# Kernel optimization log

Measured on AMD Instinct MI355X. Metric: run time of the kernel, lower is better.

The kernel has to match this reference:

```python
import jax, jax.numpy as jnp
import numpy as np

N_NODES = 100000
DIM_IN = 128
DIM_OUT = 128
N_EDGES = 1600000
EPS = 0.0  # PyG GINConv default, non-trainable


def setup_inputs() -> dict:
    key = jax.random.key(0)
    k1, k2, k3, k4, k5, k6 = jax.random.split(key, 6)
    node_feature = jax.random.normal(k1, (N_NODES, DIM_IN), dtype=jnp.float32)
    edge_index = jax.random.randint(k2, (2, N_EDGES), 0, N_NODES, dtype=jnp.int64)
    s1 = 1.0 / np.sqrt(DIM_IN)
    s2 = 1.0 / np.sqrt(DIM_OUT)
    W1 = jax.random.uniform(k3, (DIM_IN, DIM_OUT), jnp.float32, -s1, s1)
    b1 = jax.random.uniform(k4, (DIM_OUT,), jnp.float32, -s1, s1)
    W2 = jax.random.uniform(k5, (DIM_OUT, DIM_OUT), jnp.float32, -s2, s2)
    b2 = jax.random.uniform(k6, (DIM_OUT,), jnp.float32, -s2, s2)
    return {"node_feature": node_feature, "edge_index": edge_index,
            "W1": W1, "b1": b1, "W2": W2, "b2": b2}


def reference(node_feature, edge_index, W1, b1, W2, b2):
    src, dst = edge_index[0], edge_index[1]
    # scatter-add neighbor aggregation: messages x_j = x[src] summed at dst
    agg = jax.ops.segment_sum(node_feature[src], dst, num_segments=N_NODES)  # [N, d]
    h = (1.0 + EPS) * node_feature + agg
    h = jax.nn.relu(h @ W1 + b1)
    return h @ W2 + b2
```

## Files before the change

kernel.cpp:

```cpp
#include <hip/hip_runtime.h>

#define NN 100000
#define D  128
#define NE 1600000

#define NBK2 782
#define CAP2 2816
#define EPB  8192
#define NFB  196
#define ENTCAP 2048

typedef __bf16 bf16x8 __attribute__((ext_vector_type(8)));
typedef __bf16 bf16x4 __attribute__((ext_vector_type(4)));
typedef float  f32x4  __attribute__((ext_vector_type(4)));

__global__ __launch_bounds__(256)
void init_kernel(const float* __restrict__ W1, const float* __restrict__ W2,
                 __bf16* __restrict__ w1t, __bf16* __restrict__ w2t,
                 int* __restrict__ gcur) {
    const int bid = blockIdx.x;
    const int tid = threadIdx.x;
    if (bid < 128) {
        int i = bid * 256 + tid;
        if (i < 16384) {
            int c = i >> 7, k = i & 127;
            w1t[i] = (__bf16)W1[k * 128 + c];
        } else {
            int j = i - 16384;
            int c = j >> 7, k = j & 127;
            w2t[j] = (__bf16)W2[k * 128 + c];
        }
    } else {
        int i = (bid - 128) * 256 + tid;
        if (i < NBK2) gcur[i] = 0;
    }
}

__global__ __launch_bounds__(512)
void fill2x_kernel(const float* __restrict__ x, const int* __restrict__ ei,
                   int* __restrict__ gcur, __bf16* __restrict__ xb,
                   int* __restrict__ bedge) {
    __shared__ int            stage[EPB];
    __shared__ unsigned short bid16[EPB];
    __shared__ int            lofs[NBK2];
    __shared__ int            lpos[NBK2];
    __shared__ int            gbase[NBK2];
    __shared__ int            ssum[512];
    __shared__ int            tot;

    const int tid = threadIdx.x;
    const int e0  = blockIdx.x * EPB;

    for (int b = tid; b < NBK2; b += 512) lpos[b] = 0;
    __syncthreads();

    int eb[16], epk[16];
    #pragma unroll 16
    for (int k = 0; k < 16; ++k) {
        int e = e0 + k * 512 + tid;
        eb[k] = -1;
        if (e < NE) {
            int s = ei[e];
            int d = ei[NE + e];
            if ((unsigned)s < NN && (unsigned)d < NN) {
                eb[k]  = d >> 7;
                epk[k] = ((d & 127) << 17) | s;
                atomicAdd(&lpos[eb[k]], 1);
            }
        }
    }

    for (int i = blockIdx.x * 512 + tid; i < NN * 32; i += NFB * 512) {
        float4 v = reinterpret_cast<const float4*>(x)[i];
        bf16x4 o = {(__bf16)v.x, (__bf16)v.y, (__bf16)v.z, (__bf16)v.w};
        reinterpret_cast<bf16x4*>(xb)[i] = o;
    }
    __syncthreads();

    int t2 = tid * 2;
    int c0 = (t2 < NBK2) ? lpos[t2] : 0;
    int c1 = (t2 + 1 < NBK2) ? lpos[t2 + 1] : 0;
    ssum[tid] = c0 + c1;
    __syncthreads();
    for (int off = 1; off < 512; off <<= 1) {
        int v = (tid >= off) ? ssum[tid - off] : 0;
        __syncthreads();
        ssum[tid] += v;
        __syncthreads();
    }
    int excl = ssum[tid] - (c0 + c1);
    if (t2 < NBK2) {
        lofs[t2] = excl;
        lpos[t2] = excl;
        if (c0) gbase[t2] = atomicAdd(&gcur[t2], c0);
    }
    if (t2 + 1 < NBK2) {
        lofs[t2 + 1] = excl + c0;
        lpos[t2 + 1] = excl + c0;
        if (c1) gbase[t2 + 1] = atomicAdd(&gcur[t2 + 1], c1);
    }
    if (tid == 511) tot = ssum[511];
    __syncthreads();

    #pragma unroll 16
    for (int k = 0; k < 16; ++k) {
        if (eb[k] >= 0) {
            int r = atomicAdd(&lpos[eb[k]], 1);
            stage[r] = epk[k];
            bid16[r] = (unsigned short)eb[k];
        }
    }
    __syncthreads();

    int T = tot;
    for (int i = tid; i < T; i += 512) {
        int b   = bid16[i];
        int pos = gbase[b] + (i - lofs[b]);
        if (pos < CAP2) bedge[b * CAP2 + pos] = stage[i];
    }
}

__global__ __launch_bounds__(256)
void gather3_kernel(const __bf16* __restrict__ xb, const int* __restrict__ gcur,
                    const int* __restrict__ bedge, __bf16* __restrict__ hb) {
    __shared__ int ent[ENTCAP];
    __shared__ int c64[64], ofs[65], cur[64], scn[64];

    const int b    = blockIdx.x >> 1;
    const int half = blockIdx.x & 1;
    const int tid  = threadIdx.x;

    int cnt = gcur[b]; if (cnt > CAP2) cnt = CAP2;
    const int base = b * CAP2;

    if (tid < 64) c64[tid] = 0;
    __syncthreads();

    for (int i = tid; i < cnt; i += 256) {
        int v  = bedge[base + i];
        int dl = v >> 17;
        if ((dl >> 6) == half) atomicAdd(&c64[dl & 63], 1);
    }
    __syncthreads();

    if (tid < 64) scn[tid] = c64[tid];
    __syncthreads();
    #pragma unroll
    for (int off = 1; off < 64; off <<= 1) {
        int v = (tid >= off && tid < 64) ? scn[tid - off] : 0;
        __syncthreads();
        if (tid < 64) scn[tid] += v;
        __syncthreads();
    }
    if (tid < 64) {
        ofs[tid + 1] = scn[tid];
        if (tid == 0) ofs[0] = 0;
        cur[tid] = scn[tid] - c64[tid];
    }
    __syncthreads();

    for (int i = tid; i < cnt; i += 256) {
        int v  = bedge[base + i];
        int dl = v >> 17;
        if ((dl >> 6) == half) {
            int r = atomicAdd(&cur[dl & 63], 1);
            if (r < ENTCAP) ent[r] = v & 0x1FFFF;
        }
    }
    __syncthreads();

    const int wave   = tid >> 6;
    const int lane   = tid & 63;
    const int half32 = lane >> 5;
    const int l31    = lane & 31;
    const bf16x4* xv4 = reinterpret_cast<const bf16x4*>(xb);

    for (int q = wave; q < 64; q += 4) {
        int node = b * 128 + half * 64 + q;
        if (node >= NN) continue;
        int beg = ofs[q], end = ofs[q + 1];
        if (beg > ENTCAP) beg = ENTCAP;
        if (end > ENTCAP) end = ENTCAP;

        float a0 = 0.f, a1 = 0.f, a2 = 0.f, a3 = 0.f;
        float b0 = 0.f, b1 = 0.f, b2f = 0.f, b3 = 0.f;
        int j = beg;
        for (; j + 4 <= end; j += 4) {
            int s0 = ent[j + half32];
            int s1 = ent[j + 2 + half32];
            bf16x4 v0 = xv4[(size_t)s0 * 32 + l31];
            bf16x4 v1 = xv4[(size_t)s1 * 32 + l31];
            a0 += (float)v0[0]; a1 += (float)v0[1];
            a2 += (float)v0[2]; a3 += (float)v0[3];
            b0 += (float)v1[0]; b1 += (float)v1[1];
            b2f += (float)v1[2]; b3 += (float)v1[3];
        }
        if (j + 2 <= end) {
            int s0 = ent[j + half32];
            bf16x4 v0 = xv4[(size_t)s0 * 32 + l31];
            a0 += (float)v0[0]; a1 += (float)v0[1];
            a2 += (float)v0[2]; a3 += (float)v0[3];
            j += 2;
        }
        if (j < end && half32 == 0) {
            int s0 = ent[j];
            bf16x4 v0 = xv4[(size_t)s0 * 32 + l31];
            a0 += (float)v0[0]; a1 += (float)v0[1];
            a2 += (float)v0[2]; a3 += (float)v0[3];
        }
        a0 += b0; a1 += b1; a2 += b2f; a3 += b3;
        a0 += __shfl_xor(a0, 32); a1 += __shfl_xor(a1, 32);
        a2 += __shfl_xor(a2, 32); a3 += __shfl_xor(a3, 32);

        if (half32 == 0) {
            bf16x4 sv = xv4[(size_t)node * 32 + l31];
            bf16x4 o = {(__bf16)(a0 + (float)sv[0]), (__bf16)(a1 + (float)sv[1]),
                        (__bf16)(a2 + (float)sv[2]), (__bf16)(a3 + (float)sv[3])};
            reinterpret_cast<bf16x4*>(hb)[(size_t)node * 32 + l31] = o;
        }
    }
}

__global__ __launch_bounds__(512)
void mlp2_kernel(const __bf16* __restrict__ hb,
                 const __bf16* __restrict__ w1t,
                 const __bf16* __restrict__ w2t,
                 const float* __restrict__ b1,
                 const float* __restrict__ b2,
                 float* __restrict__ out) {
    __shared__ __align__(16) unsigned char sh_h[128 * 256];

    const int tid  = threadIdx.x;
    const int row0 = blockIdx.x * 128;

    for (int c = tid; c < 2048; c += 512) {
        int r = c >> 4, s = c & 15;
        int grow = row0 + r;
        int4 val = make_int4(0, 0, 0, 0);
        if (grow < NN) val = *reinterpret_cast<const int4*>(hb + (size_t)grow * 128 + s * 8);
        *reinterpret_cast<int4*>(sh_h + r * 256 + ((s * 16) ^ ((r & 7) << 4))) = val;
    }
    __syncthreads();

    const int wave  = tid >> 6;
    const int lane  = tid & 63;
    const int wr    = wave >> 2;
    const int wc    = wave & 3;
    const int l15   = lane & 15;
    const int kbyte = (lane >> 4) * 16;
    const int kelem = (lane >> 4) * 8;

    bf16x8 bf[2][4];
    #pragma unroll
    for (int nn = 0; nn < 2; ++nn) {
        int col = wc * 32 + nn * 16 + l15;
        #pragma unroll
        for (int ks = 0; ks < 4; ++ks)
            bf[nn][ks] = *reinterpret_cast<const bf16x8*>(
                w1t + col * 128 + ks * 32 + kelem);
    }

    f32x4 acc[4][2];
    #pragma unroll
    for (int m = 0; m < 4; ++m) {
        acc[m][0] = f32x4{0.f, 0.f, 0.f, 0.f};
        acc[m][1] = f32x4{0.f, 0.f, 0.f, 0.f};
        int row = wr * 64 + m * 16 + l15;
        bf16x8 af[4];
        #pragma unroll
        for (int ks = 0; ks < 4; ++ks)
            af[ks] = *reinterpret_cast<const bf16x8*>(
                sh_h + row * 256 + ((ks * 64 + kbyte) ^ ((row & 7) << 4)));
        #pragma unroll
        for (int ks = 0; ks < 4; ++ks) {
            acc[m][0] = __builtin_amdgcn_mfma_f32_16x16x32_bf16(af[ks], bf[0][ks], acc[m][0], 0, 0, 0);
            acc[m][1] = __builtin_amdgcn_mfma_f32_16x16x32_bf16(af[ks], bf[1][ks], acc[m][1], 0, 0, 0);
        }
    }

    float bias1a = b1[wc * 32 + l15];
    float bias1b = b1[wc * 32 + 16 + l15];

    __syncthreads();

    #pragma unroll
    for (int m = 0; m < 4; ++m) {
        #pragma unroll
        for (int nn = 0; nn < 2; ++nn) {
            int col = wc * 32 + nn * 16 + l15;
            float bb = nn ? bias1b : bias1a;
            #pragma unroll
            for (int j = 0; j < 4; ++j) {
                int row = wr * 64 + m * 16 + (lane >> 4) * 4 + j;
                float v = fmaxf(acc[m][nn][j] + bb, 0.f);
                *reinterpret_cast<__bf16*>(
                    sh_h + row * 256 + ((col * 2) ^ ((row & 7) << 4))) = (__bf16)v;
            }
        }
    }
    __syncthreads();

    #pragma unroll
    for (int nn = 0; nn < 2; ++nn) {
        int col = wc * 32 + nn * 16 + l15;
        #pragma unroll
        for (int ks = 0; ks < 4; ++ks)
            bf[nn][ks] = *reinterpret_cast<const bf16x8*>(
                w2t + col * 128 + ks * 32 + kelem);
    }

    f32x4 acc2[4][2];
    #pragma unroll
    for (int m = 0; m < 4; ++m) {
        acc2[m][0] = f32x4{0.f, 0.f, 0.f, 0.f};
        acc2[m][1] = f32x4{0.f, 0.f, 0.f, 0.f};
        int row = wr * 64 + m * 16 + l15;
        bf16x8 af[4];
        #pragma unroll
        for (int ks = 0; ks < 4; ++ks)
            af[ks] = *reinterpret_cast<const bf16x8*>(
                sh_h + row * 256 + ((ks * 64 + kbyte) ^ ((row & 7) << 4)));
        #pragma unroll
        for (int ks = 0; ks < 4; ++ks) {
            acc2[m][0] = __builtin_amdgcn_mfma_f32_16x16x32_bf16(af[ks], bf[0][ks], acc2[m][0], 0, 0, 0);
            acc2[m][1] = __builtin_amdgcn_mfma_f32_16x16x32_bf16(af[ks], bf[1][ks], acc2[m][1], 0, 0, 0);
        }
    }

    float bias2a = b2[wc * 32 + l15];
    float bias2b = b2[wc * 32 + 16 + l15];
    #pragma unroll
    for (int m = 0; m < 4; ++m) {
        #pragma unroll
        for (int nn = 0; nn < 2; ++nn) {
            int col = wc * 32 + nn * 16 + l15;
            float bb = nn ? bias2b : bias2a;
            #pragma unroll
            for (int j = 0; j < 4; ++j) {
                int row = row0 + wr * 64 + m * 16 + (lane >> 4) * 4 + j;
                if (row < NN) out[(size_t)row * 128 + col] = acc2[m][nn][j] + bb;
            }
        }
    }
}

extern "C" void kernel_launch(void* const* d_in, const int* in_sizes, int n_in,
                              void* d_out, int out_size, void* d_ws, size_t ws_size,
                              hipStream_t stream) {
    const float* x  = (const float*)d_in[0];
    const int*   ei = (const int*)d_in[1];
    const float* W1 = (const float*)d_in[2];
    const float* b1 = (const float*)d_in[3];
    const float* W2 = (const float*)d_in[4];
    const float* b2 = (const float*)d_in[5];
    float* out = (float*)d_out;

    int* gcur  = (int*)d_ws;
    int* bedge = gcur + NBK2;
    size_t int_end = (size_t)(NBK2 + (size_t)NBK2 * CAP2) * 4;
    size_t bf_off  = (int_end + 255) & ~(size_t)255;
    __bf16* xb  = (__bf16*)((char*)d_ws + bf_off);
    __bf16* hb  = xb + (size_t)NN * D;
    __bf16* w1t = hb + (size_t)NN * D;
    __bf16* w2t = w1t + D * D;

    init_kernel<<<132, 256, 0, stream>>>(W1, W2, w1t, w2t, gcur);
    fill2x_kernel<<<NFB, 512, 0, stream>>>(x, ei, gcur, xb, bedge);
    gather3_kernel<<<NBK2 * 2, 256, 0, stream>>>(xb, gcur, bedge, hb);
    mlp2_kernel<<<NBK2, 512, 0, stream>>>(hb, w1t, w2t, b1, b2, out);
}
```

Measured before the change: 137.5 us.

## Fuse neighbor gather with two-layer MLP in a single kernel

The gather kernel now writes each block's 64 aggregated rows straight into shared memory in the swizzled layout and runs both MFMA GEMM layers on that tile in the same block. This removes the bf16 intermediate buffer, its global write and re-read, and one kernel launch. In exchange each block holds more shared memory and registers, and it does GEMM work with only 4 waves over 64 rows, so the MLP phase may use fewer MFMA units at once and overlap less with gather latency.

After: 155.3 us. 1.13x slower.

```diff
diff --git a/kernel.cpp b/kernel.cpp
--- a/kernel.cpp
+++ b/kernel.cpp
@@ -121,10 +121,16 @@
 }
 
 __global__ __launch_bounds__(256)
-void gather3_kernel(const __bf16* __restrict__ xb, const int* __restrict__ gcur,
-                    const int* __restrict__ bedge, __bf16* __restrict__ hb) {
+void gather_mlp_kernel(const __bf16* __restrict__ xb, const int* __restrict__ gcur,
+                       const int* __restrict__ bedge,
+                       const __bf16* __restrict__ w1t,
+                       const __bf16* __restrict__ w2t,
+                       const float* __restrict__ b1,
+                       const float* __restrict__ b2,
+                       float* __restrict__ out) {
     __shared__ int ent[ENTCAP];
     __shared__ int c64[64], ofs[65], cur[64], scn[64];
+    __shared__ __align__(16) unsigned char sh_h[64 * 256];
 
     const int b    = blockIdx.x >> 1;
     const int half = blockIdx.x & 1;
@@ -177,75 +183,54 @@
 
     for (int q = wave; q < 64; q += 4) {
         int node = b * 128 + half * 64 + q;
-        if (node >= NN) continue;
-        int beg = ofs[q], end = ofs[q + 1];
-        if (beg > ENTCAP) beg = ENTCAP;
-        if (end > ENTCAP) end = ENTCAP;
-
         float a0 = 0.f, a1 = 0.f, a2 = 0.f, a3 = 0.f;
-        float b0 = 0.f, b1 = 0.f, b2f = 0.f, b3 = 0.f;
-        int j = beg;
-        for (; j + 4 <= end; j += 4) {
-            int s0 = ent[j + half32];
-            int s1 = ent[j + 2 + half32];
-            bf16x4 v0 = xv4[(size_t)s0 * 32 + l31];
-            bf16x4 v1 = xv4[(size_t)s1 * 32 + l31];
-            a0 += (float)v0[0]; a1 += (float)v0[1];
-            a2 += (float)v0[2]; a3 += (float)v0[3];
-            b0 += (float)v1[0]; b1 += (float)v1[1];
-            b2f += (float)v1[2]; b3 += (float)v1[3];
-        }
-        if (j + 2 <= end) {
-            int s0 = ent[j + half32];
-            bf16x4 v0 = xv4[(size_t)s0 * 32 + l31];
-            a0 += (float)v0[0]; a1 += (float)v0[1];
-            a2 += (float)v0[2]; a3 += (float)v0[3];
-            j += 2;
-        }
-        if (j < end && half32 == 0) {
-            int s0 = ent[j];
-            bf16x4 v0 = xv4[(size_t)s0 * 32 + l31];
-            a0 += (float)v0[0]; a1 += (float)v0[1];
-            a2 += (float)v0[2]; a3 += (float)v0[3];
-        }
-        a0 += b0; a1 += b1; a2 += b2f; a3 += b3;
-        a0 += __shfl_xor(a0, 32); a1 += __shfl_xor(a1, 32);
-        a2 += __shfl_xor(a2, 32); a3 += __shfl_xor(a3, 32);
-
+        if (node < NN) {
+            int beg = ofs[q], end = ofs[q + 1];
+            if (beg > ENTCAP) beg = ENTCAP;
+            if (end > ENTCAP) end = ENTCAP;
+            float b0 = 0.f, b1f = 0.f, b2f = 0.f, b3f = 0.f;
+            int j = beg;
+            for (; j + 4 <= end; j += 4) {
+                int s0 = ent[j + half32];
+                int s1 = ent[j + 2 + half32];
+                bf16x4 v0 = xv4[(size_t)s0 * 32 + l31];
+                bf16x4 v1 = xv4[(size_t)s1 * 32 + l31];
+                a0 += (float)v0[0]; a1 += (float)v0[1];
+                a2 += (float)v0[2]; a3 += (float)v0[3];
+                b0 += (float)v1[0]; b1f += (float)v1[1];
+                b2f += (float)v1[2]; b3f += (float)v1[3];
+            }
+            if (j + 2 <= end) {
+                int s0 = ent[j + half32];
+                bf16x4 v0 = xv4[(size_t)s0 * 32 + l31];
+                a0 += (float)v0[0]; a1 += (float)v0[1];
+                a2 += (float)v0[2]; a3 += (float)v0[3];
+                j += 2;
+            }
+            if (j < end && half32 == 0) {
+                int s0 = ent[j];
+                bf16x4 v0 = xv4[(size_t)s0 * 32 + l31];
+                a0 += (float)v0[0]; a1 += (float)v0[1];
+                a2 += (float)v0[2]; a3 += (float)v0[3];
+            }
+            a0 += b0; a1 += b1f; a2 += b2f; a3 += b3f;
+            a0 += __shfl_xor(a0, 32); a1 += __shfl_xor(a1, 32);
+            a2 += __shfl_xor(a2, 32); a3 += __shfl_xor(a3, 32);
+            if (half32 == 0) {
+                bf16x4 sv = xv4[(size_t)node * 32 + l31];
+                a0 += (float)sv[0]; a1 += (float)sv[1];
+                a2 += (float)sv[2]; a3 += (float)sv[3];
+            }
+        }
         if (half32 == 0) {
-            bf16x4 sv = xv4[(size_t)node * 32 + l31];
-            bf16x4 o = {(__bf16)(a0 + (float)sv[0]), (__bf16)(a1 + (float)sv[1]),
-                        (__bf16)(a2 + (float)sv[2]), (__bf16)(a3 + (float)sv[3])};
-            reinterpret_cast<bf16x4*>(hb)[(size_t)node * 32 + l31] = o;
-        }
-    }
-}
-
-__global__ __launch_bounds__(512)
-void mlp2_kernel(const __bf16* __restrict__ hb,
-                 const __bf16* __restrict__ w1t,
-                 const __bf16* __restrict__ w2t,
-                 const float* __restrict__ b1,
-                 const float* __restrict__ b2,
-                 float* __restrict__ out) {
-    __shared__ __align__(16) unsigned char sh_h[128 * 256];
-
-    const int tid  = threadIdx.x;
-    const int row0 = blockIdx.x * 128;
-
-    for (int c = tid; c < 2048; c += 512) {
-        int r = c >> 4, s = c & 15;
-        int grow = row0 + r;
-        int4 val = make_int4(0, 0, 0, 0);
-        if (grow < NN) val = *reinterpret_cast<const int4*>(hb + (size_t)grow * 128 + s * 8);
-        *reinterpret_cast<int4*>(sh_h + r * 256 + ((s * 16) ^ ((r & 7) << 4))) = val;
-    }
-    __syncthreads();
-
-    const int wave  = tid >> 6;
-    const int lane  = tid & 63;
-    const int wr    = wave >> 2;
-    const int wc    = wave & 3;
+            bf16x4 o = {(__bf16)a0, (__bf16)a1, (__bf16)a2, (__bf16)a3};
+            *reinterpret_cast<bf16x4*>(
+                sh_h + q * 256 + ((l31 * 8) ^ ((q & 7) << 4))) = o;
+        }
+    }
+    __syncthreads();
+
+    const int wv    = wave;
     const int l15   = lane & 15;
     const int kbyte = (lane >> 4) * 16;
     const int kelem = (lane >> 4) * 8;
@@ -253,7 +238,7 @@
     bf16x8 bf[2][4];
     #pragma unroll
     for (int nn = 0; nn < 2; ++nn) {
-        int col = wc * 32 + nn * 16 + l15;
+        int col = wv * 32 + nn * 16 + l15;
         #pragma unroll
         for (int ks = 0; ks < 4; ++ks)
             bf[nn][ks] = *reinterpret_cast<const bf16x8*>(
@@ -265,7 +250,7 @@
     for (int m = 0; m < 4; ++m) {
         acc[m][0] = f32x4{0.f, 0.f, 0.f, 0.f};
         acc[m][1] = f32x4{0.f, 0.f, 0.f, 0.f};
-        int row = wr * 64 + m * 16 + l15;
+        int row = m * 16 + l15;
         bf16x8 af[4];
         #pragma unroll
         for (int ks = 0; ks < 4; ++ks)
@@ -278,8 +263,8 @@
         }
     }
 
-    float bias1a = b1[wc * 32 + l15];
-    float bias1b = b1[wc * 32 + 16 + l15];
+    float bias1a = b1[wv * 32 + l15];
+    float bias1b = b1[wv * 32 + 16 + l15];
 
     __syncthreads();
 
@@ -287,11 +272,11 @@
     for (int m = 0; m < 4; ++m) {
         #pragma unroll
         for (int nn = 0; nn < 2; ++nn) {
-            int col = wc * 32 + nn * 16 + l15;
+            int col = wv * 32 + nn * 16 + l15;
             float bb = nn ? bias1b : bias1a;
             #pragma unroll
             for (int j = 0; j < 4; ++j) {
-                int row = wr * 64 + m * 16 + (lane >> 4) * 4 + j;
+                int row = m * 16 + (lane >> 4) * 4 + j;
                 float v = fmaxf(acc[m][nn][j] + bb, 0.f);
                 *reinterpret_cast<__bf16*>(
                     sh_h + row * 256 + ((col * 2) ^ ((row & 7) << 4))) = (__bf16)v;
@@ -302,7 +287,7 @@
 
     #pragma unroll
     for (int nn = 0; nn < 2; ++nn) {
-        int col = wc * 32 + nn * 16 + l15;
+        int col = wv * 32 + nn * 16 + l15;
         #pragma unroll
         for (int ks = 0; ks < 4; ++ks)
             bf[nn][ks] = *reinterpret_cast<const bf16x8*>(
@@ -314,7 +299,7 @@
     for (int m = 0; m < 4; ++m) {
         acc2[m][0] = f32x4{0.f, 0.f, 0.f, 0.f};
         acc2[m][1] = f32x4{0.f, 0.f, 0.f, 0.f};
-        int row = wr * 64 + m * 16 + l15;
+        int row = m * 16 + l15;
         bf16x8 af[4];
         #pragma unroll
         for (int ks = 0; ks < 4; ++ks)
@@ -327,17 +312,18 @@
         }
     }
 
-    float bias2a = b2[wc * 32 + l15];
-    float bias2b = b2[wc * 32 + 16 + l15];
+    float bias2a = b2[wv * 32 + l15];
+    float bias2b = b2[wv * 32 + 16 + l15];
+    const int row0 = b * 128 + half * 64;
     #pragma unroll
     for (int m = 0; m < 4; ++m) {
         #pragma unroll
         for (int nn = 0; nn < 2; ++nn) {
-            int col = wc * 32 + nn * 16 + l15;
+            int col = wv * 32 + nn * 16 + l15;
             float bb = nn ? bias2b : bias2a;
             #pragma unroll
             for (int j = 0; j < 4; ++j) {
-                int row = row0 + wr * 64 + m * 16 + (lane >> 4) * 4 + j;
+                int row = row0 + m * 16 + (lane >> 4) * 4 + j;
                 if (row < NN) out[(size_t)row * 128 + col] = acc2[m][nn][j] + bb;
             }
         }
@@ -360,12 +346,11 @@
     size_t int_end = (size_t)(NBK2 + (size_t)NBK2 * CAP2) * 4;
     size_t bf_off  = (int_end + 255) & ~(size_t)255;
     __bf16* xb  = (__bf16*)((char*)d_ws + bf_off);
-    __bf16* hb  = xb + (size_t)NN * D;
-    __bf16* w1t = hb + (size_t)NN * D;
+    __bf16* w1t = xb + (size_t)NN * D;
     __bf16* w2t = w1t + D * D;
 
     init_kernel<<<132, 256, 0, stream>>>(W1, W2, w1t, w2t, gcur);
     fill2x_kernel<<<NFB, 512, 0, stream>>>(x, ei, gcur, xb, bedge);
-    gather3_kernel<<<NBK2 * 2, 256, 0, stream>>>(xb, gcur, bedge, hb);
-    mlp2_kernel<<<NBK2, 512, 0, stream>>>(hb, w1t, w2t, b1, b2, out);
+    gather_mlp_kernel<<<NBK2 * 2, 256, 0, stream>>>(xb, gcur, bedge,
+                                                    w1t, w2t, b1, b2, out);
 }
```
